# Kernel optimization log

Hardware: AMD Instinct MI355X
Metric: run time of the kernel (lower is better)

Reference implementation:

```python
import jax, jax.numpy as jnp
import numpy as np

K_CENTERS = 10
G_CENTERS = 2
EPS = 1e-12  # tf.math.l2_normalize epsilon


def setup_inputs() -> dict:
    key = jax.random.key(0)
    k1, k2, k3 = jax.random.split(key, 3)
    B, H, W, D = 16, 16, 64, 512
    KC = K_CENTERS + G_CENTERS
    feat = jax.random.normal(k1, (B, H, W, D), dtype=jnp.float32)
    cluster_score = jax.random.normal(k2, (B, H, W, KC), dtype=jnp.float32)
    cluster = jax.random.normal(k3, (KC, D), dtype=jnp.float32)
    return {"feat": feat, "cluster_score": cluster_score, "cluster": cluster}


def reference(feat, cluster_score, cluster):
    B, H, W, D = feat.shape
    KC = cluster.shape[0]
    # Softmax over clusters (stable)
    A = jax.nn.softmax(cluster_score, axis=-1)            # [B,H,W,KC]
    # Flatten spatial dims: sum_{s} A[b,s,k] * (feat[b,s,d] - cluster[k,d])
    Af = A.reshape(B, H * W, KC)
    ff = feat.reshape(B, H * W, D)
    # = einsum(A, feat) - (sum_s A)[b,k] * cluster[k,d]  (avoids [B,S,KC,D] intermediate)
    cluster_res = jnp.einsum('bsk,bsd->bkd', Af, ff) - Af.sum(axis=1)[..., None] * cluster[None]
    # GhostVLAD: keep only real clusters
    cluster_res = cluster_res[:, :K_CENTERS, :]           # [B,K,D]
    # L2 normalize over feature dim
    sq = jnp.sum(cluster_res * cluster_res, axis=-1, keepdims=True)
    cluster_l2 = cluster_res * jax.lax.rsqrt(jnp.maximum(sq, EPS))
    return cluster_l2.reshape(B, K_CENTERS * D)
```

## Files before the change

kernel.cpp:

```cpp
#include <hip/hip_runtime.h>


#define B_   16
#define S_   1024
#define D_   512
#define KC_  12
#define K_   10
#define CH_  32
#define SCH_ (S_ / CH_)
#define NT   512
#define NPAR 4
#define NPX  (SCH_ / NPAR)

__global__ __launch_bounds__(NT, 4) void vlad_accum(
    const float* __restrict__ feat, const float* __restrict__ score,
    float* __restrict__ part, float* __restrict__ asum_part)
{
    const int bid = blockIdx.x;
    const int b   = bid >> 5;
    const int c   = bid & (CH_ - 1);
    const int s0  = c * SCH_;
    const int tid = threadIdx.x;
    const int par = tid >> 7;
    const int col = tid & 127;

    __shared__ float  As[SCH_][KC_];
    __shared__ float4 red[NPAR - 1][K_][128];

    if (tid < SCH_) {
        const float4* sp = (const float4*)(score + (size_t)(b * S_ + s0 + tid) * KC_);
        const float4 w0 = sp[0], w1 = sp[1], w2 = sp[2];
        float x[KC_] = {w0.x, w0.y, w0.z, w0.w, w1.x, w1.y, w1.z, w1.w,
                        w2.x, w2.y, w2.z, w2.w};
        float m = x[0];
        #pragma unroll
        for (int k = 1; k < KC_; k++) m = fmaxf(m, x[k]);
        float sum = 0.f;
        #pragma unroll
        for (int k = 0; k < KC_; k++) { x[k] = __expf(x[k] - m); sum += x[k]; }
        const float inv = 1.0f / sum;
        #pragma unroll
        for (int k = 0; k < KC_; k++) x[k] *= inv;
        *(float4*)&As[tid][0] = make_float4(x[0], x[1], x[2],  x[3]);
        *(float4*)&As[tid][4] = make_float4(x[4], x[5], x[6],  x[7]);
        *(float4*)&As[tid][8] = make_float4(x[8], x[9], x[10], x[11]);
        #pragma unroll
        for (int k = 0; k < K_; k++) {
            float r = x[k];
            r += __shfl_down(r, 16, 32);
            r += __shfl_down(r, 8, 32);
            r += __shfl_down(r, 4, 32);
            r += __shfl_down(r, 2, 32);
            r += __shfl_down(r, 1, 32);
            if (tid == 0) asum_part[(b * CH_ + c) * K_ + k] = r;
        }
    }
    __syncthreads();

    const float4* fp = (const float4*)(feat + (size_t)(b * S_ + s0) * D_) + col;
    float acc[K_][4];
    #pragma unroll
    for (int k = 0; k < K_; k++)
        acc[k][0] = acc[k][1] = acc[k][2] = acc[k][3] = 0.f;

    #pragma unroll
    for (int i = 0; i < NPX; i++) {
        const int s = i * NPAR + par;
        const float4 v  = fp[(size_t)s * 128];
        const float4 a0 = *(const float4*)&As[s][0];
        const float4 a1 = *(const float4*)&As[s][4];
        const float2 a2 = *(const float2*)&As[s][8];
        const float a[K_] = {a0.x, a0.y, a0.z, a0.w, a1.x, a1.y, a1.z, a1.w,
                             a2.x, a2.y};
        #pragma unroll
        for (int k = 0; k < K_; k++) {
            acc[k][0] += a[k] * v.x;
            acc[k][1] += a[k] * v.y;
            acc[k][2] += a[k] * v.z;
            acc[k][3] += a[k] * v.w;
        }
    }

    if (par) {
        #pragma unroll
        for (int k = 0; k < K_; k++)
            red[par - 1][k][col] =
                make_float4(acc[k][0], acc[k][1], acc[k][2], acc[k][3]);
    }
    __syncthreads();
    if (!par) {
        float* pp = part + (((size_t)(b * K_) * CH_ + c) * D_) + col * 4;
        #pragma unroll
        for (int k = 0; k < K_; k++) {
            float v0 = acc[k][0], v1 = acc[k][1], v2 = acc[k][2], v3 = acc[k][3];
            #pragma unroll
            for (int p = 0; p < NPAR - 1; p++) {
                const float4 t = red[p][k][col];
                v0 += t.x; v1 += t.y; v2 += t.z; v3 += t.w;
            }
            *(float4*)(pp + (size_t)k * CH_ * D_) = make_float4(v0, v1, v2, v3);
        }
    }
}

__global__ __launch_bounds__(NT, 4) void vlad_final(
    const float* __restrict__ part, const float* __restrict__ asum_part,
    const float* __restrict__ cluster, float* __restrict__ out)
{
    const int b    = blockIdx.x / K_;
    const int k    = blockIdx.x % K_;
    const int tid  = threadIdx.x;
    const int cg   = tid >> 7;
    const int dcol = tid & 127;
    const int lane = tid & 63;
    const int wave = tid >> 6;

    __shared__ float4 red2[3][128];
    __shared__ float  asumS;
    __shared__ float  wsum2[2];

    const float4* base =
        (const float4*)(part + (((size_t)(b * K_ + k) * CH_) + cg * 8) * D_) + dcol;
    float4 a = make_float4(0.f, 0.f, 0.f, 0.f);
    #pragma unroll
    for (int cc = 0; cc < 8; cc++) {
        const float4 v = base[(size_t)cc * 128];
        a.x += v.x; a.y += v.y; a.z += v.z; a.w += v.w;
    }

    if (tid < 32) {
        float r = asum_part[(b * CH_ + tid) * K_ + k];
        r += __shfl_down(r, 16, 32);
        r += __shfl_down(r, 8, 32);
        r += __shfl_down(r, 4, 32);
        r += __shfl_down(r, 2, 32);
        r += __shfl_down(r, 1, 32);
        if (tid == 0) asumS = r;
    }

    if (cg) red2[cg - 1][dcol] = a;
    __syncthreads();

    float4 r4;
    float  sq = 0.f;
    if (!cg) {
        const float4 r0 = red2[0][dcol], r1 = red2[1][dcol], r2 = red2[2][dcol];
        const float4 cv = ((const float4*)(cluster + (size_t)k * D_))[dcol];
        const float asv = asumS;
        r4.x = a.x + r0.x + r1.x + r2.x - asv * cv.x;
        r4.y = a.y + r0.y + r1.y + r2.y - asv * cv.y;
        r4.z = a.z + r0.z + r1.z + r2.z - asv * cv.z;
        r4.w = a.w + r0.w + r1.w + r2.w - asv * cv.w;
        sq = r4.x * r4.x + r4.y * r4.y + r4.z * r4.z + r4.w * r4.w;
        #pragma unroll
        for (int off = 32; off > 0; off >>= 1) sq += __shfl_down(sq, off, 64);
        if (lane == 0) wsum2[wave] = sq;
    }
    __syncthreads();
    if (!cg) {
        const float tot   = wsum2[0] + wsum2[1];
        const float scale = rsqrtf(fmaxf(tot, 1e-12f));
        ((float4*)(out + (size_t)(b * K_ + k) * D_))[dcol] =
            make_float4(r4.x * scale, r4.y * scale, r4.z * scale, r4.w * scale);
    }
}

extern "C" void kernel_launch(void* const* d_in, const int* in_sizes, int n_in,
                              void* d_out, int out_size, void* d_ws, size_t ws_size,
                              hipStream_t stream) {
    const float* feat    = (const float*)d_in[0];
    const float* score   = (const float*)d_in[1];
    const float* cluster = (const float*)d_in[2];
    float* out = (float*)d_out;

    float* part      = (float*)d_ws;
    float* asum_part = part + (size_t)B_ * K_ * CH_ * D_;

    vlad_accum<<<B_ * CH_, NT, 0, stream>>>(feat, score, part, asum_part);
    vlad_final<<<B_ * K_, NT, 0, stream>>>(part, asum_part, cluster, out);
}
```

Baseline: 82.38 us.

## Fuse accumulate and finalize kernels with per-batch atomic counter handoff

Merges the two kernels into one launch. Each block writes its partial sums with agent-scope atomic stores and increments a per-batch counter. The first ten blocks of each batch then spin until all 32 chunks are done and perform the reduction, cluster subtraction and L2 normalization. This removes the second launch and the gap between kernels, but adds a memset, spin-waiting and 8-byte atomic loads and stores in place of vector accesses. It also relies on all 512 blocks being co-resident to avoid deadlock.

```diff
diff --git a/kernel.cpp b/kernel.cpp
--- a/kernel.cpp
+++ b/kernel.cpp
@@ -1,4 +1,5 @@
 #include <hip/hip_runtime.h>
+#include <string.h>
 
 
 #define B_   16
@@ -12,9 +13,28 @@
 #define NPAR 4
 #define NPX  (SCH_ / NPAR)
 
-__global__ __launch_bounds__(NT, 4) void vlad_accum(
+#define PART_ELEMS ((size_t)B_ * K_ * CH_ * D_)
+
+__device__ __forceinline__ void store_f4_agent(float* p, float v0, float v1,
+                                               float v2, float v3) {
+    unsigned long long u0, u1;
+    float t0[2] = {v0, v1}, t1[2] = {v2, v3};
+    memcpy(&u0, t0, 8); memcpy(&u1, t1, 8);
+    __hip_atomic_store((unsigned long long*)p, u0,
+                       __ATOMIC_RELAXED, __HIP_MEMORY_SCOPE_AGENT);
+    __hip_atomic_store(((unsigned long long*)p) + 1, u1,
+                       __ATOMIC_RELAXED, __HIP_MEMORY_SCOPE_AGENT);
+}
+__device__ __forceinline__ float2 load_f2_agent(const float* p) {
+    unsigned long long u = __hip_atomic_load((const unsigned long long*)p,
+                                             __ATOMIC_RELAXED, __HIP_MEMORY_SCOPE_AGENT);
+    float2 v; memcpy(&v, &u, 8); return v;
+}
+
+__global__ __launch_bounds__(NT, 4) void vlad_all(
     const float* __restrict__ feat, const float* __restrict__ score,
-    float* __restrict__ part, float* __restrict__ asum_part)
+    const float* __restrict__ cluster, float* __restrict__ out,
+    int* __restrict__ ctr, float* __restrict__ part, float* __restrict__ asum_part)
 {
     const int bid = blockIdx.x;
     const int b   = bid >> 5;
@@ -23,9 +43,14 @@
     const int tid = threadIdx.x;
     const int par = tid >> 7;
     const int col = tid & 127;
+    const int lane = tid & 63;
+    const int wave = tid >> 6;
 
     __shared__ float  As[SCH_][KC_];
     __shared__ float4 red[NPAR - 1][K_][128];
+    __shared__ float4 red2[3][128];
+    __shared__ float  asumS;
+    __shared__ float  wsum2[2];
 
     if (tid < SCH_) {
         const float4* sp = (const float4*)(score + (size_t)(b * S_ + s0 + tid) * KC_);
@@ -52,7 +77,9 @@
             r += __shfl_down(r, 4, 32);
             r += __shfl_down(r, 2, 32);
             r += __shfl_down(r, 1, 32);
-            if (tid == 0) asum_part[(b * CH_ + c) * K_ + k] = r;
+            if (tid == 0)
+                __hip_atomic_store(&asum_part[(b * CH_ + c) * K_ + k], r,
+                                   __ATOMIC_RELAXED, __HIP_MEMORY_SCOPE_AGENT);
         }
     }
     __syncthreads();
@@ -98,70 +125,73 @@
                 const float4 t = red[p][k][col];
                 v0 += t.x; v1 += t.y; v2 += t.z; v3 += t.w;
             }
-            *(float4*)(pp + (size_t)k * CH_ * D_) = make_float4(v0, v1, v2, v3);
-        }
-    }
-}
-
-__global__ __launch_bounds__(NT, 4) void vlad_final(
-    const float* __restrict__ part, const float* __restrict__ asum_part,
-    const float* __restrict__ cluster, float* __restrict__ out)
-{
-    const int b    = blockIdx.x / K_;
-    const int k    = blockIdx.x % K_;
-    const int tid  = threadIdx.x;
-    const int cg   = tid >> 7;
-    const int dcol = tid & 127;
-    const int lane = tid & 63;
-    const int wave = tid >> 6;
-
-    __shared__ float4 red2[3][128];
-    __shared__ float  asumS;
-    __shared__ float  wsum2[2];
-
-    const float4* base =
-        (const float4*)(part + (((size_t)(b * K_ + k) * CH_) + cg * 8) * D_) + dcol;
-    float4 a = make_float4(0.f, 0.f, 0.f, 0.f);
-    #pragma unroll
-    for (int cc = 0; cc < 8; cc++) {
-        const float4 v = base[(size_t)cc * 128];
-        a.x += v.x; a.y += v.y; a.z += v.z; a.w += v.w;
-    }
-
-    if (tid < 32) {
-        float r = asum_part[(b * CH_ + tid) * K_ + k];
-        r += __shfl_down(r, 16, 32);
-        r += __shfl_down(r, 8, 32);
-        r += __shfl_down(r, 4, 32);
-        r += __shfl_down(r, 2, 32);
-        r += __shfl_down(r, 1, 32);
-        if (tid == 0) asumS = r;
-    }
-
-    if (cg) red2[cg - 1][dcol] = a;
+            store_f4_agent(pp + (size_t)k * CH_ * D_, v0, v1, v2, v3);
+        }
+    }
     __syncthreads();
-
-    float4 r4;
-    float  sq = 0.f;
-    if (!cg) {
-        const float4 r0 = red2[0][dcol], r1 = red2[1][dcol], r2 = red2[2][dcol];
-        const float4 cv = ((const float4*)(cluster + (size_t)k * D_))[dcol];
-        const float asv = asumS;
-        r4.x = a.x + r0.x + r1.x + r2.x - asv * cv.x;
-        r4.y = a.y + r0.y + r1.y + r2.y - asv * cv.y;
-        r4.z = a.z + r0.z + r1.z + r2.z - asv * cv.z;
-        r4.w = a.w + r0.w + r1.w + r2.w - asv * cv.w;
-        sq = r4.x * r4.x + r4.y * r4.y + r4.z * r4.z + r4.w * r4.w;
-        #pragma unroll
-        for (int off = 32; off > 0; off >>= 1) sq += __shfl_down(sq, off, 64);
-        if (lane == 0) wsum2[wave] = sq;
-    }
-    __syncthreads();
-    if (!cg) {
-        const float tot   = wsum2[0] + wsum2[1];
-        const float scale = rsqrtf(fmaxf(tot, 1e-12f));
-        ((float4*)(out + (size_t)(b * K_ + k) * D_))[dcol] =
-            make_float4(r4.x * scale, r4.y * scale, r4.z * scale, r4.w * scale);
+    if (tid == 0) {
+        __threadfence();
+        atomicAdd(&ctr[b], 1);
+    }
+
+    if ((bid & 31) < K_) {
+        const int b2 = bid >> 5;
+        const int k2 = bid & 31;
+        if (tid == 0) {
+            while (__hip_atomic_load(&ctr[b2], __ATOMIC_ACQUIRE,
+                                     __HIP_MEMORY_SCOPE_AGENT) < CH_)
+                __builtin_amdgcn_s_sleep(8);
+        }
+        __syncthreads();
+
+        const int cg   = tid >> 7;
+        const int dcol = tid & 127;
+
+        const float* base =
+            part + (((size_t)(b2 * K_ + k2) * CH_) + cg * 8) * D_ + dcol * 4;
+        float4 a = make_float4(0.f, 0.f, 0.f, 0.f);
+        #pragma unroll
+        for (int cc = 0; cc < 8; cc++) {
+            const float2 lo = load_f2_agent(base + (size_t)cc * D_);
+            const float2 hi = load_f2_agent(base + (size_t)cc * D_ + 2);
+            a.x += lo.x; a.y += lo.y; a.z += hi.x; a.w += hi.y;
+        }
+
+        if (tid < CH_) {
+            float r = __hip_atomic_load(&asum_part[(b2 * CH_ + tid) * K_ + k2],
+                                        __ATOMIC_RELAXED, __HIP_MEMORY_SCOPE_AGENT);
+            r += __shfl_down(r, 16, 32);
+            r += __shfl_down(r, 8, 32);
+            r += __shfl_down(r, 4, 32);
+            r += __shfl_down(r, 2, 32);
+            r += __shfl_down(r, 1, 32);
+            if (tid == 0) asumS = r;
+        }
+        if (cg) red2[cg - 1][dcol] = a;
+        __syncthreads();
+
+        float4 r4;
+        float  sq = 0.f;
+        if (!cg) {
+            const float4 r0 = red2[0][dcol], r1 = red2[1][dcol], r2 = red2[2][dcol];
+            const float4 cv = ((const float4*)(cluster + (size_t)k2 * D_))[dcol];
+            const float asv = asumS;
+            r4.x = a.x + r0.x + r1.x + r2.x - asv * cv.x;
+            r4.y = a.y + r0.y + r1.y + r2.y - asv * cv.y;
+            r4.z = a.z + r0.z + r1.z + r2.z - asv * cv.z;
+            r4.w = a.w + r0.w + r1.w + r2.w - asv * cv.w;
+            sq = r4.x * r4.x + r4.y * r4.y + r4.z * r4.z + r4.w * r4.w;
+            #pragma unroll
+            for (int off = 32; off > 0; off >>= 1) sq += __shfl_down(sq, off, 64);
+            if (lane == 0) wsum2[wave] = sq;
+        }
+        __syncthreads();
+        if (!cg) {
+            const float tot   = wsum2[0] + wsum2[1];
+            const float scale = rsqrtf(fmaxf(tot, 1e-12f));
+            ((float4*)(out + (size_t)(b2 * K_ + k2) * D_))[dcol] =
+                make_float4(r4.x * scale, r4.y * scale, r4.z * scale, r4.w * scale);
+        }
     }
 }
 
@@ -173,9 +203,11 @@
     const float* cluster = (const float*)d_in[2];
     float* out = (float*)d_out;
 
-    float* part      = (float*)d_ws;
-    float* asum_part = part + (size_t)B_ * K_ * CH_ * D_;
-
-    vlad_accum<<<B_ * CH_, NT, 0, stream>>>(feat, score, part, asum_part);
-    vlad_final<<<B_ * K_, NT, 0, stream>>>(part, asum_part, cluster, out);
-}
+    int*   ctr       = (int*)d_ws;
+    float* part      = (float*)((char*)d_ws + 256);
+    float* asum_part = part + PART_ELEMS;
+
+    hipMemsetAsync(ctr, 0, 64, stream);
+    vlad_all<<<B_ * CH_, NT, 0, stream>>>(feat, score, cluster, out,
+                                          ctr, part, asum_part);
+}
```

Result: slower. 117.3 us (+42.4%).
